# Performance work log

Hardware: AMD Instinct MI355X
Metric: run time of the kernel (lower is better)

Reference implementation:

```python
import jax, jax.numpy as jnp
import numpy as np

N = 50000    # nodes
E = 600000   # edges
F = 128      # num_features
ED = 16      # edge_dim
H = 4        # heads
D = 32       # per-head channels = hidden_units // heads
HID = H * D  # hidden_units = 128
C = 10       # num_classes


def _lin(k, fan_in, fan_out):
    # torch.nn.Linear-style init scale
    return jax.random.uniform(k, (fan_in, fan_out), jnp.float32, -1.0, 1.0) / np.sqrt(fan_in)


def setup_inputs() -> dict:
    key = jax.random.key(0)
    ks = jax.random.split(key, 24)
    inp = {
        "x": jax.random.normal(ks[0], (N, F), jnp.float32),
        "edge_index": jax.random.randint(ks[1], (2, E), 0, N, dtype=jnp.int32),
        "edge_attr": jax.random.normal(ks[2], (E, ED), jnp.float32),
    }
    j = 3
    for l, ind in enumerate([F, HID]):
        specs = {"q": (ind, HID, True), "k": (ind, HID, True), "v": (ind, HID, True),
                 "e": (ED, HID, False), "s": (ind, HID, True)}
        for nm, (i, o, bias) in specs.items():
            inp[f"W{nm}{l}"] = _lin(ks[j], i, o); j += 1
            if bias:
                inp[f"b{nm}{l}"] = jnp.zeros((o,), jnp.float32)
    inp["Wout"] = _lin(ks[j], HID, C)
    inp["bout"] = jnp.zeros((C,), jnp.float32)
    return inp


def _transformer_conv(x, src, dst, eattr, Wq, bq, Wk, bk, Wv, bv, We, Ws, bs):
    # PyG TransformerConv: concat=True, root_weight=True, beta=False, eval dropout.
    n = x.shape[0]
    q = (x @ Wq + bq).reshape(n, H, D)
    k = (x @ Wk + bk).reshape(n, H, D)
    v = (x @ Wv + bv).reshape(n, H, D)
    e = (eattr @ We).reshape(-1, H, D)           # edge embedding, added to key and value
    kj = k[src] + e                              # [E, H, D]
    vj = v[src] + e                              # [E, H, D]
    logits = jnp.einsum("ehd,ehd->eh", q[dst], kj) / np.sqrt(D)
    m = jax.ops.segment_max(logits, dst, num_segments=n)          # [N, H]
    ex = jnp.exp(logits - m[dst])
    denom = jax.ops.segment_sum(ex, dst, num_segments=n)          # [N, H]
    alpha = ex / (denom[dst] + 1e-16)                             # PyG softmax eps
    out = jax.ops.segment_sum(vj * alpha[..., None], dst, num_segments=n)
    return out.reshape(n, HID) + x @ Ws + bs                      # concat heads + skip


def reference(x, edge_index, edge_attr,
              Wq0, bq0, Wk0, bk0, Wv0, bv0, We0, Ws0, bs0,
              Wq1, bq1, Wk1, bk1, Wv1, bv1, We1, Ws1, bs1,
              Wout, bout):
    src, dst = edge_index[0], edge_index[1]
    h = jax.nn.relu(_transformer_conv(x, src, dst, edge_attr,
                                      Wq0, bq0, Wk0, bk0, Wv0, bv0, We0, Ws0, bs0))
    h = jax.nn.relu(_transformer_conv(h, src, dst, edge_attr,
                                      Wq1, bq1, Wk1, bk1, Wv1, bv1, We1, Ws1, bs1))
    logits = h @ Wout + bout
    return jax.nn.log_softmax(logits, axis=1)
```

## Files before the change

### kernel.cpp

```cpp
#include <hip/hip_runtime.h>

typedef unsigned short u16;
typedef unsigned int u32;
typedef __attribute__((ext_vector_type(4))) u16 u16x4;
typedef __attribute__((ext_vector_type(8))) u16 u16x8;
typedef __attribute__((ext_vector_type(4))) u32 u32x4;
typedef __attribute__((ext_vector_type(8))) short short8;
typedef __attribute__((ext_vector_type(4))) float f32x4;
typedef __attribute__((ext_vector_type(4))) float f4;
typedef __attribute__((ext_vector_type(2))) float f2;

#define NN 50000
#define NE 600000
#define HEADS 4
#define DH 32
#define HIDU 128
#define NC 10
#define NBLK 196
#define WES_T 34
#define WES_H 546

#define SCALE2 0.25503486164f

__device__ __forceinline__ float bf2f(u16 u) {
    union { unsigned int i; float f; } c; c.i = ((unsigned int)u) << 16; return c.f;
}
__device__ __forceinline__ u16 f2bf(float f) {
    union { float f; unsigned int i; } c; c.f = f;
    unsigned int x = c.i;
    return (u16)((x + 0x7fffu + ((x >> 16) & 1u)) >> 16);
}
__device__ __forceinline__ float lo_bf(u32 d) { return __uint_as_float(d << 16); }
__device__ __forceinline__ float hi_bf(u32 d) { return __uint_as_float(d & 0xffff0000u); }
__device__ __forceinline__ float qadd_xor1(float v) {
    int o = __builtin_amdgcn_update_dpp(0, __float_as_int(v), 0xB1, 0xF, 0xF, true);
    return v + __int_as_float(o);
}
__device__ __forceinline__ float qadd_xor2(float v) {
    int o = __builtin_amdgcn_update_dpp(0, __float_as_int(v), 0x4E, 0xF, 0xF, true);
    return v + __int_as_float(o);
}

__global__ void k_zero(int* p, int n) {
    int i = blockIdx.x * blockDim.x + threadIdx.x;
    if (i < n) p[i] = 0;
}

__global__ void k_hist(const int* __restrict__ dst, int* __restrict__ deg) {
    int i = blockIdx.x * blockDim.x + threadIdx.x;
    if (i < NE) atomicAdd(&deg[dst[i]], 1);
}

__global__ __launch_bounds__(256) void scan_a(const int* __restrict__ deg,
                                              int* __restrict__ bsum) {
    __shared__ int red[4];
    int i = blockIdx.x * 256 + threadIdx.x;
    int v = (i < NN) ? deg[i] : 0;
    #pragma unroll
    for (int off = 1; off < 64; off <<= 1) v += __shfl_xor(v, off);
    if ((threadIdx.x & 63) == 0) red[threadIdx.x >> 6] = v;
    __syncthreads();
    if (threadIdx.x == 0) bsum[blockIdx.x] = red[0] + red[1] + red[2] + red[3];
}

__global__ __launch_bounds__(256) void scan_b(const int* __restrict__ bsum,
                                              int* __restrict__ boff,
                                              int* __restrict__ row_ptr) {
    __shared__ int s[256];
    int t = threadIdx.x;
    int v = (t < NBLK) ? bsum[t] : 0;
    s[t] = v;
    __syncthreads();
    for (int off = 1; off < 256; off <<= 1) {
        int x = (t >= off) ? s[t - off] : 0;
        __syncthreads();
        s[t] += x;
        __syncthreads();
    }
    if (t < NBLK) boff[t] = s[t] - v;
    if (t == 0) row_ptr[NN] = NE;
}

__global__ __launch_bounds__(256) void scan_c(const int* __restrict__ deg,
                                              const int* __restrict__ boff,
                                              int* __restrict__ row_ptr,
                                              int* __restrict__ cursor) {
    __shared__ int s[256];
    int t = threadIdx.x;
    int i = blockIdx.x * 256 + t;
    int v = (i < NN) ? deg[i] : 0;
    s[t] = v;
    __syncthreads();
    for (int off = 1; off < 256; off <<= 1) {
        int x = (t >= off) ? s[t - off] : 0;
        __syncthreads();
        s[t] += x;
        __syncthreads();
    }
    if (i < NN) {
        int r = boff[blockIdx.x] + s[t] - v;
        row_ptr[i] = r;
        cursor[i] = r;
    }
}

__global__ void k_scatter(const int* __restrict__ ei, const float* __restrict__ eattr,
                          int* __restrict__ cursor,
                          int* __restrict__ csr_src, u16* __restrict__ ea16) {
    int i = blockIdx.x * blockDim.x + threadIdx.x;
    if (i < NE) {
        int s = ei[i];
        int d = ei[NE + i];
        int pos = atomicAdd(&cursor[d], 1);
        csr_src[pos] = s;
        const f4* ep = (const f4*)(eattr + (size_t)i * 16);
        f4 a = ep[0], b = ep[1], c = ep[2], dd = ep[3];
        u16x8 o0, o1;
        #pragma unroll
        for (int j = 0; j < 4; j++) {
            o0[j] = f2bf(a[j]); o0[4 + j] = f2bf(b[j]);
            o1[j] = f2bf(c[j]); o1[4 + j] = f2bf(dd[j]);
        }
        *(u16x8*)(ea16 + (size_t)pos * 16)     = o0;
        *(u16x8*)(ea16 + (size_t)pos * 16 + 8) = o1;
    }
}

__global__ void k_cvtw(const float* w0, const float* w1, const float* w2, const float* w3,
                       const float* w4, const float* w5, const float* w6, const float* w7,
                       u16* __restrict__ hi) {
    const float* w;
    switch (blockIdx.x) {
        case 0: w = w0; break; case 1: w = w1; break;
        case 2: w = w2; break; case 3: w = w3; break;
        case 4: w = w4; break; case 5: w = w5; break;
        case 6: w = w6; break; default: w = w7; break;
    }
    u16* oh = hi + blockIdx.x * 16384;
    #pragma unroll
    for (int i = 0; i < 8; i++) {
        int idx = threadIdx.x + (blockIdx.y * 8 + i) * 256;
        int k = idx >> 7, n = idx & 127;
        oh[n * 128 + k] = f2bf(w[idx]);
    }
}

template<int XB>
__global__ __launch_bounds__(256) void gemm4(
    const void* __restrict__ Xv, const u16* __restrict__ WtHi,
    const float* __restrict__ b0, const float* __restrict__ b1,
    const float* __restrict__ b2, const float* __restrict__ b3,
    float* __restrict__ outq, u16* __restrict__ outk, u16* __restrict__ outv,
    float* __restrict__ outs, int nrows)
{
    __shared__ u16 Bs[128 * 128];
    const float* Xf = (const float*)Xv;
    const u16*   Xh = (const u16*)Xv;

    const int wave = threadIdx.x >> 6, lane = threadIdx.x & 63;
    const int n0 = lane & 15;
    const int qw = lane >> 4;
    const int kq = qw * 8;

    short8 ah[2][4];
    #pragma unroll
    for (int rt = 0; rt < 2; rt++) {
        int arow = blockIdx.x * 128 + wave * 32 + rt * 16 + n0;
        int arow_c = arow < nrows ? arow : nrows - 1;
        size_t xbase = (size_t)arow_c * HIDU + kq;
        #pragma unroll
        for (int ks = 0; ks < 4; ks++) {
            if (XB) {
                ah[rt][ks] = *(const short8*)(Xh + xbase + ks * 32);
            } else {
                f4 a0 = *(const f4*)(Xf + xbase + ks * 32);
                f4 a1 = *(const f4*)(Xf + xbase + ks * 32 + 4);
                #pragma unroll
                for (int j = 0; j < 4; j++) {
                    ah[rt][ks][j]     = (short)(__float_as_uint(a0[j]) >> 16);
                    ah[rt][ks][4 + j] = (short)(__float_as_uint(a1[j]) >> 16);
                }
            }
        }
    }

    #pragma unroll
    for (int mat = 0; mat < 4; mat++) {
        if (mat > 0) __syncthreads();
        const u16* wh = WtHi + mat * 16384;
        #pragma unroll
        for (int i = 0; i < 8; i++) {
            int idx = threadIdx.x + i * 256;
            int n = idx >> 4, g = idx & 15;
            *(u16x8*)(&Bs[n * 128 + ((g ^ (n & 15)) << 3)]) = *(const u16x8*)(wh + n * 128 + g * 8);
        }
        __syncthreads();

        f32x4 acc[2][8];
        #pragma unroll
        for (int rt = 0; rt < 2; rt++)
            #pragma unroll
            for (int nt = 0; nt < 8; nt++) acc[rt][nt] = (f32x4){0.f, 0.f, 0.f, 0.f};

        #pragma unroll
        for (int ks = 0; ks < 4; ks++) {
            #pragma unroll
            for (int nt = 0; nt < 8; nt++) {
                const int boff = (nt * 16 + n0) * 128 + (((ks << 2) + qw) ^ n0) * 8;
                short8 bh = *(const short8*)(&Bs[boff]);
                #pragma unroll
                for (int rt = 0; rt < 2; rt++)
                    acc[rt][nt] = __builtin_amdgcn_mfma_f32_16x16x32_bf16(ah[rt][ks], bh, acc[rt][nt], 0, 0, 0);
            }
        }

        const float* bia = (mat == 0) ? b0 : (mat == 1) ? b1 : (mat == 2) ? b2 : b3;
        #pragma unroll
        for (int rt = 0; rt < 2; rt++) {
            const int rbase = blockIdx.x * 128 + wave * 32 + rt * 16 + qw * 4;
            #pragma unroll
            for (int nt = 0; nt < 8; nt++) {
                int col = nt * 16 + n0;
                float bv = bia[col];
                #pragma unroll
                for (int r = 0; r < 4; r++) {
                    int grow = rbase + r;
                    if (grow < nrows) {
                        float v = acc[rt][nt][r] + bv;
                        if (mat == 0)      outq[(size_t)grow * HIDU + col] = v;
                        else if (mat == 1) outk[(size_t)grow * HIDU + col] = f2bf(v);
                        else if (mat == 2) outv[(size_t)grow * HIDU + col] = f2bf(v);
                        else               outs[(size_t)grow * HIDU + col] = v;
                    }
                }
            }
        }
    }
}

template<int MODE>
__global__ __launch_bounds__(256) void attn_t(
    const float* __restrict__ qb, const u16* __restrict__ kb, const u16* __restrict__ vb,
    const float* __restrict__ sb, const u16* __restrict__ ea16, const float* __restrict__ We,
    const int* __restrict__ row_ptr, const int* __restrict__ csr_src,
    u16* __restrict__ hout_b16,
    const float* __restrict__ Wout, const float* __restrict__ bout,
    float* __restrict__ out_logits)
{
    __shared__ float WeS[4 * WES_H];
    __shared__ float WoT[MODE ? (NC * HIDU) : 1];
    __shared__ float boS[MODE ? NC : 1];

    #pragma unroll
    for (int i = 0; i < 8; i++) {
        int idx = threadIdx.x + i * 256;
        int tt = idx >> 7, c = idx & 127;
        int h = c >> 5, j = c & 31;
        WeS[h * WES_H + tt * WES_T + j] = We[idx];
    }
    if (MODE == 1) {
        #pragma unroll
        for (int i = 0; i < 5; i++) {
            int idx = threadIdx.x + i * 256;
            if (idx < HIDU * NC) {
                int c = idx >> 7, ch = idx & 127;
                WoT[idx] = Wout[ch * NC + c];
            }
        }
        if (threadIdx.x < NC) boS[threadIdx.x] = bout[threadIdx.x];
    }
    __syncthreads();

    int gtid = blockIdx.x * 256 + threadIdx.x;
    int n   = gtid >> 4;
    int l16 = gtid & 15;
    int h   = l16 >> 2;
    int sub = l16 & 3;
    const int lane = threadIdx.x & 63;
    const float* WeH = &WeS[h * WES_H];
    const int j0  = sub * 8;
    const int ch0 = h * DH + j0;
    const int t0  = sub * 4;

    f4 qa, qbv;
    {
        const f4* qp = (const f4*)(qb + (size_t)n * HIDU + ch0);
        qa = qp[0]; qbv = qp[1];
    }

    f4 g4v;
    {
        float part[16];
        #pragma unroll
        for (int t = 0; t < 16; t++) {
            const f2* wp = (const f2*)(WeH + t * WES_T + j0);
            f2 w0 = wp[0], w1 = wp[1], w2 = wp[2], w3 = wp[3];
            part[t] = qa[0] * w0.x + qa[1] * w0.y + qa[2] * w1.x + qa[3] * w1.y
                    + qbv[0] * w2.x + qbv[1] * w2.y + qbv[2] * w3.x + qbv[3] * w3.y;
        }
        #pragma unroll
        for (int t = 0; t < 16; t++) { part[t] = qadd_xor1(part[t]); part[t] = qadd_xor2(part[t]); }
        g4v[0] = part[t0]; g4v[1] = part[t0 + 1]; g4v[2] = part[t0 + 2]; g4v[3] = part[t0 + 3];
    }

    float l = 0.f;
    f4 O0 = {0.f, 0.f, 0.f, 0.f}, O1 = {0.f, 0.f, 0.f, 0.f};
    f4 a4 = {0.f, 0.f, 0.f, 0.f};

    const int r0 = row_ptr[n], r1 = row_ptr[n + 1];

    for (int e = r0; e < r1; e += 4) {
        const int e1 = (e + 1 < r1) ? e + 1 : e;
        const int e2 = (e + 2 < r1) ? e + 2 : e;
        const int e3 = (e + 3 < r1) ? e + 3 : e;
        int s0 = csr_src[e], s1 = csr_src[e1], s2 = csr_src[e2], s3 = csr_src[e3];
        u32 eo0 = (u32)e  * 16u + t0, eo1 = (u32)e1 * 16u + t0;
        u32 eo2 = (u32)e2 * 16u + t0, eo3 = (u32)e3 * 16u + t0;
        u16x4 x0 = *(const u16x4*)(ea16 + eo0);
        u16x4 x1 = *(const u16x4*)(ea16 + eo1);
        u16x4 x2 = *(const u16x4*)(ea16 + eo2);
        u16x4 x3 = *(const u16x4*)(ea16 + eo3);
        u32 ko0 = (u32)s0 * 128u + ch0, ko1 = (u32)s1 * 128u + ch0;
        u32 ko2 = (u32)s2 * 128u + ch0, ko3 = (u32)s3 * 128u + ch0;
        u32x4 k0 = *(const u32x4*)(kb + ko0);
        u32x4 k1 = *(const u32x4*)(kb + ko1);
        u32x4 k2 = *(const u32x4*)(kb + ko2);
        u32x4 k3 = *(const u32x4*)(kb + ko3);
        u32x4 v0 = *(const u32x4*)(vb + ko0);
        u32x4 v1 = *(const u32x4*)(vb + ko1);
        u32x4 v2 = *(const u32x4*)(vb + ko2);
        u32x4 v3 = *(const u32x4*)(vb + ko3);

        f4 ea0 = {bf2f(x0[0]), bf2f(x0[1]), bf2f(x0[2]), bf2f(x0[3])};
        f4 ea1 = {bf2f(x1[0]), bf2f(x1[1]), bf2f(x1[2]), bf2f(x1[3])};
        f4 ea2 = {bf2f(x2[0]), bf2f(x2[1]), bf2f(x2[2]), bf2f(x2[3])};
        f4 ea3 = {bf2f(x3[0]), bf2f(x3[1]), bf2f(x3[2]), bf2f(x3[3])};

        f4 ac0 = qa * (f4){lo_bf(k0[0]), hi_bf(k0[0]), lo_bf(k0[1]), hi_bf(k0[1])}
               + qbv * (f4){lo_bf(k0[2]), hi_bf(k0[2]), lo_bf(k0[3]), hi_bf(k0[3])}
               + g4v * ea0;
        f4 ac1 = qa * (f4){lo_bf(k1[0]), hi_bf(k1[0]), lo_bf(k1[1]), hi_bf(k1[1])}
               + qbv * (f4){lo_bf(k1[2]), hi_bf(k1[2]), lo_bf(k1[3]), hi_bf(k1[3])}
               + g4v * ea1;
        f4 ac2 = qa * (f4){lo_bf(k2[0]), hi_bf(k2[0]), lo_bf(k2[1]), hi_bf(k2[1])}
               + qbv * (f4){lo_bf(k2[2]), hi_bf(k2[2]), lo_bf(k2[3]), hi_bf(k2[3])}
               + g4v * ea2;
        f4 ac3 = qa * (f4){lo_bf(k3[0]), hi_bf(k3[0]), lo_bf(k3[1]), hi_bf(k3[1])}
               + qbv * (f4){lo_bf(k3[2]), hi_bf(k3[2]), lo_bf(k3[3]), hi_bf(k3[3])}
               + g4v * ea3;
        float d0 = (ac0[0] + ac0[1]) + (ac0[2] + ac0[3]);
        float d1 = (ac1[0] + ac1[1]) + (ac1[2] + ac1[3]);
        float d2 = (ac2[0] + ac2[1]) + (ac2[2] + ac2[3]);
        float d3 = (ac3[0] + ac3[1]) + (ac3[2] + ac3[3]);
        d0 = qadd_xor1(d0); d1 = qadd_xor1(d1); d2 = qadd_xor1(d2); d3 = qadd_xor1(d3);
        d0 = qadd_xor2(d0); d1 = qadd_xor2(d1); d2 = qadd_xor2(d2); d3 = qadd_xor2(d3);

        float w0 = exp2f(d0 * SCALE2);
        float w1 = (e + 1 < r1) ? exp2f(d1 * SCALE2) : 0.f;
        float w2 = (e + 2 < r1) ? exp2f(d2 * SCALE2) : 0.f;
        float w3 = (e + 3 < r1) ? exp2f(d3 * SCALE2) : 0.f;
        l += (w0 + w1) + (w2 + w3);

        O0 = O0
           + (f4){lo_bf(v0[0]), hi_bf(v0[0]), lo_bf(v0[1]), hi_bf(v0[1])} * w0
           + (f4){lo_bf(v1[0]), hi_bf(v1[0]), lo_bf(v1[1]), hi_bf(v1[1])} * w1
           + (f4){lo_bf(v2[0]), hi_bf(v2[0]), lo_bf(v2[1]), hi_bf(v2[1])} * w2
           + (f4){lo_bf(v3[0]), hi_bf(v3[0]), lo_bf(v3[1]), hi_bf(v3[1])} * w3;
        O1 = O1
           + (f4){lo_bf(v0[2]), hi_bf(v0[2]), lo_bf(v0[3]), hi_bf(v0[3])} * w0
           + (f4){lo_bf(v1[2]), hi_bf(v1[2]), lo_bf(v1[3]), hi_bf(v1[3])} * w1
           + (f4){lo_bf(v2[2]), hi_bf(v2[2]), lo_bf(v2[3]), hi_bf(v2[3])} * w2
           + (f4){lo_bf(v3[2]), hi_bf(v3[2]), lo_bf(v3[3]), hi_bf(v3[3])} * w3;
        a4 = a4 + ea0 * w0 + ea1 * w1 + ea2 * w2 + ea3 * w3;
    }

    float af[16];
    #pragma unroll
    for (int t = 0; t < 16; t++)
        af[t] = __shfl(a4[t & 3], (lane & ~3) | (t >> 2));

    float invl = 1.0f / (l + 1e-16f);
    const f4* sp = (const f4*)(sb + (size_t)n * HIDU + ch0);
    f4 sp0 = sp[0], sp1 = sp[1];

    f4 evA = {0.f, 0.f, 0.f, 0.f}, evB = {0.f, 0.f, 0.f, 0.f};
    #pragma unroll
    for (int t = 0; t < 16; t++) {
        float a = af[t];
        const f2* wp = (const f2*)(WeH + t * WES_T + j0);
        f2 w0 = wp[0], w1 = wp[1], w2 = wp[2], w3 = wp[3];
        evA[0] += a * w0.x; evA[1] += a * w0.y; evA[2] += a * w1.x; evA[3] += a * w1.y;
        evB[0] += a * w2.x; evB[1] += a * w2.y; evB[2] += a * w3.x; evB[3] += a * w3.y;
    }

    f4 val0, val1;
    #pragma unroll
    for (int j = 0; j < 4; j++) {
        val0[j] = fmaxf((O0[j] + evA[j]) * invl + sp0[j], 0.f);
        val1[j] = fmaxf((O1[j] + evB[j]) * invl + sp1[j], 0.f);
    }

    if (MODE == 0) {
        u16x8 hv;
        #pragma unroll
        for (int j = 0; j < 4; j++) { hv[j] = f2bf(val0[j]); hv[4 + j] = f2bf(val1[j]); }
        *(u16x8*)(hout_b16 + (u32)n * 128u + ch0) = hv;
    } else {
        float plg[NC];
        #pragma unroll
        for (int c = 0; c < NC; c++) {
            const f4* wr = (const f4*)(WoT + c * HIDU + ch0);
            f4 wa = wr[0], wb = wr[1];
            plg[c] = val0[0] * wa[0] + val0[1] * wa[1] + val0[2] * wa[2] + val0[3] * wa[3]
                   + val1[0] * wb[0] + val1[1] * wb[1] + val1[2] * wb[2] + val1[3] * wb[3];
        }
        #pragma unroll
        for (int mask = 1; mask < 16; mask <<= 1) {
            #pragma unroll
            for (int c = 0; c < NC; c++) plg[c] += __shfl_xor(plg[c], mask);
        }
        float lg[NC];
        float mx = -INFINITY;
        #pragma unroll
        for (int c = 0; c < NC; c++) { lg[c] = plg[c] + boS[c]; mx = fmaxf(mx, lg[c]); }
        float sum = 0.f;
        #pragma unroll
        for (int c = 0; c < NC; c++) sum += __expf(lg[c] - mx);
        float lse = mx + __logf(sum);
        if (l16 < NC) out_logits[(size_t)n * NC + l16] = lg[l16] - lse;
    }
}

extern "C" void kernel_launch(void* const* d_in, const int* in_sizes, int n_in,
                              void* d_out, int out_size, void* d_ws, size_t ws_size,
                              hipStream_t stream) {
    const float* x     = (const float*)d_in[0];
    const int*   ei    = (const int*)d_in[1];
    const float* eattr = (const float*)d_in[2];
    const float *Wq0 = (const float*)d_in[3],  *bq0 = (const float*)d_in[4];
    const float *Wk0 = (const float*)d_in[5],  *bk0 = (const float*)d_in[6];
    const float *Wv0 = (const float*)d_in[7],  *bv0 = (const float*)d_in[8];
    const float *We0 = (const float*)d_in[9];
    const float *Ws0 = (const float*)d_in[10], *bs0 = (const float*)d_in[11];
    const float *Wq1 = (const float*)d_in[12], *bq1 = (const float*)d_in[13];
    const float *Wk1 = (const float*)d_in[14], *bk1 = (const float*)d_in[15];
    const float *Wv1 = (const float*)d_in[16], *bv1 = (const float*)d_in[17];
    const float *We1 = (const float*)d_in[18];
    const float *Ws1 = (const float*)d_in[19], *bs1 = (const float*)d_in[20];
    const float *Wout = (const float*)d_in[21], *bout = (const float*)d_in[22];

    char* p = (char*)d_ws;
    auto alloc = [&](size_t bytes) -> void* {
        void* r = (void*)p;
        p += (bytes + 255) & ~(size_t)255;
        return r;
    };
    int* deg      = (int*)alloc(NN * 4);
    int* row_ptr  = (int*)alloc((NN + 1) * 4);
    int* cursor   = (int*)alloc(NN * 4);
    int* bsum     = (int*)alloc(NBLK * 4);
    int* boff     = (int*)alloc(NBLK * 4);
    int* csr_src  = (int*)alloc((size_t)NE * 4);
    float* qb     = (float*)alloc((size_t)NN * HIDU * 4);
    u16* kb       = (u16*)alloc((size_t)NN * HIDU * 2);
    u16* vb       = (u16*)alloc((size_t)NN * HIDU * 2);
    float* sbuf   = (float*)alloc((size_t)NN * HIDU * 4);
    u16* hb16     = (u16*)alloc((size_t)NN * HIDU * 2);
    u16* ea16     = (u16*)alloc((size_t)NE * 16 * 2);
    u16* wthi     = (u16*)alloc(8 * 16384 * 2);

    k_zero<<<(NN + 255) / 256, 256, 0, stream>>>(deg, NN);
    k_hist<<<(NE + 255) / 256, 256, 0, stream>>>(ei + NE, deg);
    scan_a<<<NBLK, 256, 0, stream>>>(deg, bsum);
    scan_b<<<1, 256, 0, stream>>>(bsum, boff, row_ptr);
    scan_c<<<NBLK, 256, 0, stream>>>(deg, boff, row_ptr, cursor);
    k_scatter<<<(NE + 255) / 256, 256, 0, stream>>>(ei, eattr, cursor, csr_src, ea16);

    k_cvtw<<<dim3(8, 8), 256, 0, stream>>>(Wq0, Wk0, Wv0, Ws0, Wq1, Wk1, Wv1, Ws1, wthi);

    const int gm = (NN + 127) / 128;
    const int ga = (NN * 16) / 256;

    gemm4<0><<<gm, 256, 0, stream>>>(x, wthi, bq0, bk0, bv0, bs0,
                                     qb, kb, vb, sbuf, NN);
    attn_t<0><<<ga, 256, 0, stream>>>(qb, kb, vb, sbuf, ea16, We0, row_ptr, csr_src,
                                      hb16, nullptr, nullptr, nullptr);
    gemm4<1><<<gm, 256, 0, stream>>>(hb16, wthi + 4 * 16384, bq1, bk1, bv1, bs1,
                                     qb, kb, vb, sbuf, NN);
    attn_t<1><<<ga, 256, 0, stream>>>(qb, kb, vb, sbuf, ea16, We1, row_ptr, csr_src,
                                      nullptr, Wout, bout, (float*)d_out);
}
```

Baseline: 397.2 us.

## Fuse CSR build and weight conversion into one cooperative kernel

Replaces seven small preprocessing launches (zero, histogram, three scan stages, scatter, weight conversion) with a single cooperative kernel of 196 blocks that separates the phases with grid-wide syncs. The aim is to cut launch overhead and inter-kernel gaps. In exchange, the histogram and scatter phases now run on only 196 blocks with grid-stride loops, so less parallelism is available for the atomic-heavy edge passes, and each grid sync has its own cost.

Result: slower. 533.0 us (+34.2%).

```diff
diff --git a/kernel.cpp b/kernel.cpp
--- a/kernel.cpp
+++ b/kernel.cpp
@@ -1,4 +1,7 @@
 #include <hip/hip_runtime.h>
+#include <hip/hip_cooperative_groups.h>
+
+namespace cg = cooperative_groups;
 
 typedef unsigned short u16;
 typedef unsigned int u32;
@@ -41,78 +44,88 @@
     return v + __int_as_float(o);
 }
 
-__global__ void k_zero(int* p, int n) {
-    int i = blockIdx.x * blockDim.x + threadIdx.x;
-    if (i < n) p[i] = 0;
-}
-
-__global__ void k_hist(const int* __restrict__ dst, int* __restrict__ deg) {
-    int i = blockIdx.x * blockDim.x + threadIdx.x;
-    if (i < NE) atomicAdd(&deg[dst[i]], 1);
-}
-
-__global__ __launch_bounds__(256) void scan_a(const int* __restrict__ deg,
-                                              int* __restrict__ bsum) {
+__global__ __launch_bounds__(256) void k_prep(
+    const int* __restrict__ ei, const float* __restrict__ eattr,
+    const float* w0, const float* w1, const float* w2, const float* w3,
+    const float* w4, const float* w5, const float* w6, const float* w7,
+    int* __restrict__ deg, int* __restrict__ bsum, int* __restrict__ boff,
+    int* __restrict__ row_ptr, int* __restrict__ cursor,
+    int* __restrict__ csr_src, u16* __restrict__ ea16, u16* __restrict__ wthi)
+{
+    cg::grid_group grid = cg::this_grid();
+    __shared__ int s[256];
     __shared__ int red[4];
-    int i = blockIdx.x * 256 + threadIdx.x;
-    int v = (i < NN) ? deg[i] : 0;
-    #pragma unroll
-    for (int off = 1; off < 64; off <<= 1) v += __shfl_xor(v, off);
-    if ((threadIdx.x & 63) == 0) red[threadIdx.x >> 6] = v;
-    __syncthreads();
-    if (threadIdx.x == 0) bsum[blockIdx.x] = red[0] + red[1] + red[2] + red[3];
-}
-
-__global__ __launch_bounds__(256) void scan_b(const int* __restrict__ bsum,
-                                              int* __restrict__ boff,
-                                              int* __restrict__ row_ptr) {
-    __shared__ int s[256];
-    int t = threadIdx.x;
-    int v = (t < NBLK) ? bsum[t] : 0;
-    s[t] = v;
-    __syncthreads();
-    for (int off = 1; off < 256; off <<= 1) {
-        int x = (t >= off) ? s[t - off] : 0;
+    const int t = threadIdx.x;
+    const int tid = blockIdx.x * 256 + t;
+    const int NT = NBLK * 256;
+
+    if (tid < NN) deg[tid] = 0;
+    for (int idx = tid; idx < 8 * 16384; idx += NT) {
+        int mat = idx >> 14;
+        int r   = idx & 16383;
+        int k = r >> 7, n = r & 127;
+        const float* w;
+        switch (mat) {
+            case 0: w = w0; break; case 1: w = w1; break;
+            case 2: w = w2; break; case 3: w = w3; break;
+            case 4: w = w4; break; case 5: w = w5; break;
+            case 6: w = w6; break; default: w = w7; break;
+        }
+        wthi[mat * 16384 + n * 128 + k] = f2bf(w[r]);
+    }
+    grid.sync();
+
+    for (int e = tid; e < NE; e += NT) atomicAdd(&deg[ei[NE + e]], 1);
+    grid.sync();
+
+    {
+        int v = (tid < NN) ? deg[tid] : 0;
+        #pragma unroll
+        for (int off = 1; off < 64; off <<= 1) v += __shfl_xor(v, off);
+        if ((t & 63) == 0) red[t >> 6] = v;
         __syncthreads();
-        s[t] += x;
+        if (t == 0) bsum[blockIdx.x] = red[0] + red[1] + red[2] + red[3];
+    }
+    grid.sync();
+
+    if (blockIdx.x == 0) {
+        int v = (t < NBLK) ? bsum[t] : 0;
+        s[t] = v;
         __syncthreads();
-    }
-    if (t < NBLK) boff[t] = s[t] - v;
-    if (t == 0) row_ptr[NN] = NE;
-}
-
-__global__ __launch_bounds__(256) void scan_c(const int* __restrict__ deg,
-                                              const int* __restrict__ boff,
-                                              int* __restrict__ row_ptr,
-                                              int* __restrict__ cursor) {
-    __shared__ int s[256];
-    int t = threadIdx.x;
-    int i = blockIdx.x * 256 + t;
-    int v = (i < NN) ? deg[i] : 0;
-    s[t] = v;
-    __syncthreads();
-    for (int off = 1; off < 256; off <<= 1) {
-        int x = (t >= off) ? s[t - off] : 0;
+        for (int off = 1; off < 256; off <<= 1) {
+            int x = (t >= off) ? s[t - off] : 0;
+            __syncthreads();
+            s[t] += x;
+            __syncthreads();
+        }
+        if (t < NBLK) boff[t] = s[t] - v;
+        if (t == 0) row_ptr[NN] = NE;
+    }
+    grid.sync();
+
+    {
+        int v = (tid < NN) ? deg[tid] : 0;
+        s[t] = v;
         __syncthreads();
-        s[t] += x;
-        __syncthreads();
-    }
-    if (i < NN) {
-        int r = boff[blockIdx.x] + s[t] - v;
-        row_ptr[i] = r;
-        cursor[i] = r;
-    }
-}
-
-__global__ void k_scatter(const int* __restrict__ ei, const float* __restrict__ eattr,
-                          int* __restrict__ cursor,
-                          int* __restrict__ csr_src, u16* __restrict__ ea16) {
-    int i = blockIdx.x * blockDim.x + threadIdx.x;
-    if (i < NE) {
-        int s = ei[i];
-        int d = ei[NE + i];
+        for (int off = 1; off < 256; off <<= 1) {
+            int x = (t >= off) ? s[t - off] : 0;
+            __syncthreads();
+            s[t] += x;
+            __syncthreads();
+        }
+        if (tid < NN) {
+            int r = boff[blockIdx.x] + s[t] - v;
+            row_ptr[tid] = r;
+            cursor[tid] = r;
+        }
+    }
+    grid.sync();
+
+    for (int i = tid; i < NE; i += NT) {
+        int sN = ei[i];
+        int d  = ei[NE + i];
         int pos = atomicAdd(&cursor[d], 1);
-        csr_src[pos] = s;
+        csr_src[pos] = sN;
         const f4* ep = (const f4*)(eattr + (size_t)i * 16);
         f4 a = ep[0], b = ep[1], c = ep[2], dd = ep[3];
         u16x8 o0, o1;
@@ -123,25 +136,6 @@
         }
         *(u16x8*)(ea16 + (size_t)pos * 16)     = o0;
         *(u16x8*)(ea16 + (size_t)pos * 16 + 8) = o1;
-    }
-}
-
-__global__ void k_cvtw(const float* w0, const float* w1, const float* w2, const float* w3,
-                       const float* w4, const float* w5, const float* w6, const float* w7,
-                       u16* __restrict__ hi) {
-    const float* w;
-    switch (blockIdx.x) {
-        case 0: w = w0; break; case 1: w = w1; break;
-        case 2: w = w2; break; case 3: w = w3; break;
-        case 4: w = w4; break; case 5: w = w5; break;
-        case 6: w = w6; break; default: w = w7; break;
-    }
-    u16* oh = hi + blockIdx.x * 16384;
-    #pragma unroll
-    for (int i = 0; i < 8; i++) {
-        int idx = threadIdx.x + (blockIdx.y * 8 + i) * 256;
-        int k = idx >> 7, n = idx & 127;
-        oh[n * 128 + k] = f2bf(w[idx]);
     }
 }
 
@@ -434,9 +428,9 @@
 extern "C" void kernel_launch(void* const* d_in, const int* in_sizes, int n_in,
                               void* d_out, int out_size, void* d_ws, size_t ws_size,
                               hipStream_t stream) {
-    const float* x     = (const float*)d_in[0];
     const int*   ei    = (const int*)d_in[1];
     const float* eattr = (const float*)d_in[2];
+    const float* x     = (const float*)d_in[0];
     const float *Wq0 = (const float*)d_in[3],  *bq0 = (const float*)d_in[4];
     const float *Wk0 = (const float*)d_in[5],  *bk0 = (const float*)d_in[6];
     const float *Wv0 = (const float*)d_in[7],  *bv0 = (const float*)d_in[8];
@@ -469,14 +463,16 @@
     u16* ea16     = (u16*)alloc((size_t)NE * 16 * 2);
     u16* wthi     = (u16*)alloc(8 * 16384 * 2);
 
-    k_zero<<<(NN + 255) / 256, 256, 0, stream>>>(deg, NN);
-    k_hist<<<(NE + 255) / 256, 256, 0, stream>>>(ei + NE, deg);
-    scan_a<<<NBLK, 256, 0, stream>>>(deg, bsum);
-    scan_b<<<1, 256, 0, stream>>>(bsum, boff, row_ptr);
-    scan_c<<<NBLK, 256, 0, stream>>>(deg, boff, row_ptr, cursor);
-    k_scatter<<<(NE + 255) / 256, 256, 0, stream>>>(ei, eattr, cursor, csr_src, ea16);
-
-    k_cvtw<<<dim3(8, 8), 256, 0, stream>>>(Wq0, Wk0, Wv0, Ws0, Wq1, Wk1, Wv1, Ws1, wthi);
+    {
+        void* args[] = {
+            (void*)&ei, (void*)&eattr,
+            (void*)&Wq0, (void*)&Wk0, (void*)&Wv0, (void*)&Ws0,
+            (void*)&Wq1, (void*)&Wk1, (void*)&Wv1, (void*)&Ws1,
+            (void*)&deg, (void*)&bsum, (void*)&boff, (void*)&row_ptr,
+            (void*)&cursor, (void*)&csr_src, (void*)&ea16, (void*)&wthi
+        };
+        hipLaunchCooperativeKernel((void*)k_prep, dim3(NBLK), dim3(256), args, 0, stream);
+    }
 
     const int gm = (NN + 127) / 128;
     const int ga = (NN * 16) / 256;
```

## Fuse CSR build and weight conversion into one cooperative persistent kernel

Applied to the files above, without the earlier changes.

Replaces seven small preprocessing launches (zeroing, histogram, three-stage scan, scatter, weight conversion) with a single cooperative kernel that uses grid-wide syncs between phases. The grid size comes from an occupancy query, capped at a fixed maximum. If the cooperative launch fails, it falls back to a multi-launch path that merges zeroing and weight conversion into one kernel. The aim is to remove launch gaps and per-kernel overheads. The cost is the grid.sync barriers and grid-stride loops, which may do per-phase work less efficiently than the tuned separate launches.

After: 921.6 us. 132% more time.

```diff
diff --git a/kernel.cpp b/kernel.cpp
--- a/kernel.cpp
+++ b/kernel.cpp
@@ -1,4 +1,7 @@
 #include <hip/hip_runtime.h>
+#include <hip/hip_cooperative_groups.h>
+
+namespace cg = cooperative_groups;
 
 typedef unsigned short u16;
 typedef unsigned int u32;
@@ -17,6 +20,7 @@
 #define HIDU 128
 #define NC 10
 #define NBLK 196
+#define PREPB_CAP 1792
 #define WES_T 34
 #define WES_H 546
 
@@ -41,9 +45,124 @@
     return v + __int_as_float(o);
 }
 
-__global__ void k_zero(int* p, int n) {
-    int i = blockIdx.x * blockDim.x + threadIdx.x;
-    if (i < n) p[i] = 0;
+__global__ __launch_bounds__(256) void k_prep(
+    const int* __restrict__ ei, const float* __restrict__ eattr,
+    const float* w0, const float* w1, const float* w2, const float* w3,
+    const float* w4, const float* w5, const float* w6, const float* w7,
+    int* __restrict__ deg, int* __restrict__ bsum, int* __restrict__ boff,
+    int* __restrict__ row_ptr, int* __restrict__ cursor,
+    int* __restrict__ csr_src, u16* __restrict__ ea16, u16* __restrict__ wthi)
+{
+    cg::grid_group grid = cg::this_grid();
+    __shared__ int s[256];
+    __shared__ int red[4];
+    const int t = threadIdx.x;
+    const int gid = blockIdx.x * 256 + t;
+    const int gsz = gridDim.x * 256;
+
+    for (int i = gid; i < NN; i += gsz) deg[i] = 0;
+    for (int idx = gid; idx < 8 * 16384; idx += gsz) {
+        int mat = idx >> 14;
+        int r   = idx & 16383;
+        int k = r >> 7, n = r & 127;
+        const float* w;
+        switch (mat) {
+            case 0: w = w0; break; case 1: w = w1; break;
+            case 2: w = w2; break; case 3: w = w3; break;
+            case 4: w = w4; break; case 5: w = w5; break;
+            case 6: w = w6; break; default: w = w7; break;
+        }
+        wthi[mat * 16384 + n * 128 + k] = f2bf(w[r]);
+    }
+    grid.sync();
+
+    for (int e = gid; e < NE; e += gsz) atomicAdd(&deg[ei[NE + e]], 1);
+    grid.sync();
+
+    for (int c = blockIdx.x; c < NBLK; c += gridDim.x) {
+        int i = c * 256 + t;
+        int v = (i < NN) ? deg[i] : 0;
+        #pragma unroll
+        for (int off = 1; off < 64; off <<= 1) v += __shfl_xor(v, off);
+        if ((t & 63) == 0) red[t >> 6] = v;
+        __syncthreads();
+        if (t == 0) bsum[c] = red[0] + red[1] + red[2] + red[3];
+        __syncthreads();
+    }
+    grid.sync();
+
+    if (blockIdx.x == 0) {
+        int v = (t < NBLK) ? bsum[t] : 0;
+        s[t] = v;
+        __syncthreads();
+        for (int off = 1; off < 256; off <<= 1) {
+            int x = (t >= off) ? s[t - off] : 0;
+            __syncthreads();
+            s[t] += x;
+            __syncthreads();
+        }
+        if (t < NBLK) boff[t] = s[t] - v;
+        if (t == 0) row_ptr[NN] = NE;
+    }
+    grid.sync();
+
+    for (int c = blockIdx.x; c < NBLK; c += gridDim.x) {
+        int i = c * 256 + t;
+        int v = (i < NN) ? deg[i] : 0;
+        s[t] = v;
+        __syncthreads();
+        for (int off = 1; off < 256; off <<= 1) {
+            int x = (t >= off) ? s[t - off] : 0;
+            __syncthreads();
+            s[t] += x;
+            __syncthreads();
+        }
+        if (i < NN) {
+            int r = boff[c] + s[t] - v;
+            row_ptr[i] = r;
+            cursor[i] = r;
+        }
+        __syncthreads();
+    }
+    grid.sync();
+
+    for (int i = gid; i < NE; i += gsz) {
+        int sN = ei[i];
+        int d  = ei[NE + i];
+        int pos = atomicAdd(&cursor[d], 1);
+        csr_src[pos] = sN;
+        const f4* ep = (const f4*)(eattr + (size_t)i * 16);
+        f4 a = ep[0], b = ep[1], c2 = ep[2], dd = ep[3];
+        u16x8 o0, o1;
+        #pragma unroll
+        for (int j = 0; j < 4; j++) {
+            o0[j] = f2bf(a[j]); o0[4 + j] = f2bf(b[j]);
+            o1[j] = f2bf(c2[j]); o1[4 + j] = f2bf(dd[j]);
+        }
+        *(u16x8*)(ea16 + (size_t)pos * 16)     = o0;
+        *(u16x8*)(ea16 + (size_t)pos * 16 + 8) = o1;
+    }
+}
+
+__global__ void k_zcvt(const float* w0, const float* w1, const float* w2, const float* w3,
+                       const float* w4, const float* w5, const float* w6, const float* w7,
+                       int* __restrict__ deg, u16* __restrict__ wthi) {
+    int gid = blockIdx.x * 256 + threadIdx.x;
+    int gsz = gridDim.x * 256;
+    for (int i = gid; i < NN; i += gsz) deg[i] = 0;
+    for (int idx = gid; idx < 8 * 16384; idx += gsz) {
+        int mat = idx >> 14;
+        int r   = idx & 16383;
+        int k = r >> 7, n = r & 127;
+        const float* w;
+        switch (mat) {
+            case 0: w = w0; break; case 1: w = w1; break;
+            case 2: w = w2; break; case 3: w = w3; break;
+            case 4: w = w4; break; case 5: w = w5; break;
+            case 6: w = w6; break; default: w = w7; break;
+        }
+        wthi[mat * 16384 + n * 128 + k] = f2bf(w[r]);
+    }
 }
 
 __global__ void k_hist(const int* __restrict__ dst, int* __restrict__ deg) {
@@ -109,10 +228,10 @@
                           int* __restrict__ csr_src, u16* __restrict__ ea16) {
     int i = blockIdx.x * blockDim.x + threadIdx.x;
     if (i < NE) {
-        int s = ei[i];
+        int sN = ei[i];
         int d = ei[NE + i];
         int pos = atomicAdd(&cursor[d], 1);
-        csr_src[pos] = s;
+        csr_src[pos] = sN;
         const f4* ep = (const f4*)(eattr + (size_t)i * 16);
         f4 a = ep[0], b = ep[1], c = ep[2], dd = ep[3];
         u16x8 o0, o1;
@@ -123,25 +242,6 @@
         }
         *(u16x8*)(ea16 + (size_t)pos * 16)     = o0;
         *(u16x8*)(ea16 + (size_t)pos * 16 + 8) = o1;
-    }
-}
-
-__global__ void k_cvtw(const float* w0, const float* w1, const float* w2, const float* w3,
-                       const float* w4, const float* w5, const float* w6, const float* w7,
-                       u16* __restrict__ hi) {
-    const float* w;
-    switch (blockIdx.x) {
-        case 0: w = w0; break; case 1: w = w1; break;
-        case 2: w = w2; break; case 3: w = w3; break;
-        case 4: w = w4; break; case 5: w = w5; break;
-        case 6: w = w6; break; default: w = w7; break;
-    }
-    u16* oh = hi + blockIdx.x * 16384;
-    #pragma unroll
-    for (int i = 0; i < 8; i++) {
-        int idx = threadIdx.x + (blockIdx.y * 8 + i) * 256;
-        int k = idx >> 7, n = idx & 127;
-        oh[n * 128 + k] = f2bf(w[idx]);
     }
 }
 
@@ -434,9 +534,9 @@
 extern "C" void kernel_launch(void* const* d_in, const int* in_sizes, int n_in,
                               void* d_out, int out_size, void* d_ws, size_t ws_size,
                               hipStream_t stream) {
-    const float* x     = (const float*)d_in[0];
     const int*   ei    = (const int*)d_in[1];
     const float* eattr = (const float*)d_in[2];
+    const float* x     = (const float*)d_in[0];
     const float *Wq0 = (const float*)d_in[3],  *bq0 = (const float*)d_in[4];
     const float *Wk0 = (const float*)d_in[5],  *bk0 = (const float*)d_in[6];
     const float *Wv0 = (const float*)d_in[7],  *bv0 = (const float*)d_in[8];
@@ -469,14 +569,47 @@
     u16* ea16     = (u16*)alloc((size_t)NE * 16 * 2);
     u16* wthi     = (u16*)alloc(8 * 16384 * 2);
 
-    k_zero<<<(NN + 255) / 256, 256, 0, stream>>>(deg, NN);
-    k_hist<<<(NE + 255) / 256, 256, 0, stream>>>(ei + NE, deg);
-    scan_a<<<NBLK, 256, 0, stream>>>(deg, bsum);
-    scan_b<<<1, 256, 0, stream>>>(bsum, boff, row_ptr);
-    scan_c<<<NBLK, 256, 0, stream>>>(deg, boff, row_ptr, cursor);
-    k_scatter<<<(NE + 255) / 256, 256, 0, stream>>>(ei, eattr, cursor, csr_src, ea16);
-
-    k_cvtw<<<dim3(8, 8), 256, 0, stream>>>(Wq0, Wk0, Wv0, Ws0, Wq1, Wk1, Wv1, Ws1, wthi);
+    static int g_prep_grid = -1;
+    if (g_prep_grid < 0) {
+        int maxb = 0;
+        hipError_t qe = hipOccupancyMaxActiveBlocksPerMultiprocessor(&maxb, k_prep, 256, 0);
+        if (qe != hipSuccess || maxb < 1) {
+            g_prep_grid = NBLK;
+        } else {
+            long g = (long)maxb * 256;
+            if (g > PREPB_CAP) g = PREPB_CAP;
+            if (g < NBLK) g = NBLK;
+            g_prep_grid = (int)g;
+        }
+        (void)hipGetLastError();
+    }
+
+    bool coop_done = false;
+    if (g_prep_grid > 0) {
+        void* args[] = {
+            (void*)&ei, (void*)&eattr,
+            (void*)&Wq0, (void*)&Wk0, (void*)&Wv0, (void*)&Ws0,
+            (void*)&Wq1, (void*)&Wk1, (void*)&Wv1, (void*)&Ws1,
+            (void*)&deg, (void*)&bsum, (void*)&boff, (void*)&row_ptr,
+            (void*)&cursor, (void*)&csr_src, (void*)&ea16, (void*)&wthi
+        };
+        hipError_t le = hipLaunchCooperativeKernel((void*)k_prep, dim3(g_prep_grid),
+                                                   dim3(256), args, 0, stream);
+        if (le == hipSuccess) {
+            coop_done = true;
+        } else {
+            (void)hipGetLastError();
+            g_prep_grid = 0;
+        }
+    }
+    if (!coop_done) {
+        k_zcvt<<<512, 256, 0, stream>>>(Wq0, Wk0, Wv0, Ws0, Wq1, Wk1, Wv1, Ws1, deg, wthi);
+        k_hist<<<(NE + 255) / 256, 256, 0, stream>>>(ei + NE, deg);
+        scan_a<<<NBLK, 256, 0, stream>>>(deg, bsum);
+        scan_b<<<1, 256, 0, stream>>>(bsum, boff, row_ptr);
+        scan_c<<<NBLK, 256, 0, stream>>>(deg, boff, row_ptr, cursor);
+        k_scatter<<<(NE + 255) / 256, 256, 0, stream>>>(ei, eattr, cursor, csr_src, ea16);
+    }
 
     const int gm = (NN + 127) / 128;
     const int ga = (NN * 16) / 256;
```
